# Kernel optimization log

Hardware: AMD Instinct MI355X
Metric: run time of the kernel (lower is better)

The kernel has to match this reference:

```python
import jax, jax.numpy as jnp
import numpy as np

B, S, E, H = 4, 2048, 1024, 16
D = E // H  # head_dim


def setup_inputs() -> dict:
    key = jax.random.key(0)
    ks = jax.random.split(key, 5)
    scale = 1.0 / np.sqrt(E)
    return {
        "qkv": jax.random.normal(ks[0], (B, S, E), jnp.float32),
        "in_w": jax.random.normal(ks[1], (3 * E, E), jnp.float32) * scale,
        "in_b": jax.random.normal(ks[2], (3 * E,), jnp.float32) * scale,
        "out_w": jax.random.normal(ks[3], (E, E), jnp.float32) * scale,
        "out_b": jax.random.normal(ks[4], (E,), jnp.float32) * scale,
    }


def reference(qkv, in_w, in_b, out_w, out_b):
    # in_proj: torch Linear -> x @ W^T + b, output [B,S,3E]
    x1 = jnp.einsum('bse,fe->bsf', qkv, in_w) + in_b
    q, k, v = jnp.split(x1, 3, axis=2)  # each [B,S,E]
    # reshape to heads: [B,H,S,D] (contiguous head_dim slices == reshape)
    q = q.reshape(B, S, H, D).transpose(0, 2, 1, 3)
    k = k.reshape(B, S, H, D).transpose(0, 2, 1, 3)
    v = v.reshape(B, S, H, D).transpose(0, 2, 1, 3)
    scores = jnp.einsum('bhqd,bhkd->bhqk', q, k) / jnp.sqrt(jnp.float32(D))
    attn = jax.nn.softmax(scores, axis=-1)  # dropout p=0.0 -> identity
    out = jnp.einsum('bhqk,bhkd->bhqd', attn, v)  # [B,H,S,D]
    out = out.transpose(0, 2, 1, 3).reshape(B, S, E)
    return jnp.einsum('bse,fe->bsf', out, out_w) + out_b
```

## Files before the change

### kernel.cpp

```cpp
#include <hip/hip_runtime.h>


typedef __attribute__((ext_vector_type(8))) short s16x8;
typedef __attribute__((ext_vector_type(8))) __bf16 bf16x8;
typedef __attribute__((ext_vector_type(4))) float f32x4;
typedef __attribute__((ext_vector_type(16))) float f32x16;
typedef __attribute__((ext_vector_type(4))) unsigned short u16x4;
typedef __attribute__((ext_vector_type(4))) unsigned int u32x4;

#define QSCALE_F 0.18033688011112042f

#if __has_builtin(__builtin_amdgcn_exp2f)
#define EXP2F(x) __builtin_amdgcn_exp2f(x)
#else
#define EXP2F(x) exp2f(x)
#endif

__device__ __forceinline__ unsigned short f2bf(float f) {
  unsigned int u = __builtin_bit_cast(unsigned int, f);
  u += 0x7fffu + ((u >> 16) & 1u);
  return (unsigned short)(u >> 16);
}

__device__ __forceinline__ f32x4 mfma16(s16x8 a, s16x8 b, f32x4 c) {
  return __builtin_amdgcn_mfma_f32_16x16x32_bf16(
      __builtin_bit_cast(bf16x8, a), __builtin_bit_cast(bf16x8, b), c, 0, 0, 0);
}
__device__ __forceinline__ f32x16 mfma32(s16x8 a, s16x8 b, f32x16 c) {
  return __builtin_amdgcn_mfma_f32_32x32x16_bf16(
      __builtin_bit_cast(bf16x8, a), __builtin_bit_cast(bf16x8, b), c, 0, 0, 0);
}

__device__ __forceinline__ unsigned cvtpk(float lo, float hi) {
  unsigned r;
  asm("v_cvt_pk_bf16_f32 %0, %1, %2" : "=v"(r) : "v"(lo), "v"(hi));
  return r;
}
__device__ __forceinline__ void p32swap(unsigned &a, unsigned &b) {
  asm volatile("v_permlane32_swap_b32 %0, %1" : "+v"(a), "+v"(b));
}

#define GLL16(gp, lp) __builtin_amdgcn_global_load_lds(                       \
    (const __attribute__((address_space(1))) void*)(gp),                      \
    (__attribute__((address_space(3))) void*)(lp), 16, 0, 0)

#define SBAR0 __builtin_amdgcn_sched_barrier(0)
#define HWBAR __builtin_amdgcn_s_barrier()
#define LGKM0 asm volatile("s_waitcnt lgkmcnt(0)" ::: "memory")
#define VMC4 asm volatile("s_waitcnt vmcnt(4)" ::: "memory")
#define VMC0 asm volatile("s_waitcnt vmcnt(0)" ::: "memory")
#define PRIO1 __builtin_amdgcn_s_setprio(1)
#define PRIO0 __builtin_amdgcn_s_setprio(0)

__global__ void cvt_f32_bf16(const float* __restrict__ in,
                             unsigned short* __restrict__ out,
                             int n, int scale_n) {
  int idx = (blockIdx.x * 256 + threadIdx.x) * 4;
  int stride = gridDim.x * 256 * 4;
  for (int i = idx; i < n; i += stride) {
    const float4 v = *reinterpret_cast<const float4*>(in + i);
    const float sc = (i < scale_n) ? QSCALE_F : 1.0f;
    u16x4 r;
    r.x = f2bf(v.x * sc); r.y = f2bf(v.y * sc);
    r.z = f2bf(v.z * sc); r.w = f2bf(v.w * sc);
    *reinterpret_cast<u16x4*>(out + i) = r;
  }
}

__global__ __launch_bounds__(512, 2) void gemm1_8ph(
    const unsigned short* __restrict__ A, const unsigned short* __restrict__ B,
    const float* __restrict__ bias, unsigned short* __restrict__ C,
    int M, int N, int K, int qscale_cols) {
  __shared__ __align__(16) unsigned short As[2][256 * 64];
  __shared__ __align__(16) unsigned short Bs[2][256 * 64];
  const int NT = K >> 6;
  const int id = blockIdx.x;
  const int mi_ = (id & 7) * 4 + ((id >> 3) & 3);
  const int ni_ = id >> 5;
  const int bm = mi_ * 256, bn = ni_ * 256;

  const int tid = threadIdx.x;
  const int lane = tid & 63, w = tid >> 6;
  const int l15 = lane & 15, l4 = (lane >> 4) & 3;
  const int wm = w >> 2, wn = w & 3;
  const int swz = (l15 & 7) << 4;

#define STG_HALF(ldsc_, gb_, ktel_) {                                         \
    _Pragma("unroll") for (int s_ = 0; s_ < 2; ++s_) {                        \
      const int o = (w * 2 + s_) * 1024 + lane * 16;                          \
      const int row_ = o >> 7;                                                \
      const int cb_ = (o & 127) ^ ((row_ & 7) << 4);                          \
      GLL16((gb_) + (size_t)row_ * K + (ktel_) + (cb_ >> 1),                  \
            (char*)(ldsc_) + o);                                              \
    }                                                                         \
  }
#define RD_A(buf_, qm_, dst_) {                                               \
    _Pragma("unroll") for (int mt = 0; mt < 4; ++mt)                          \
      _Pragma("unroll") for (int kk = 0; kk < 2; ++kk)                        \
        dst_[mt][kk] = *(const s16x8*)((const char*)As[buf_] +                \
            (wm * 128 + (qm_) * 64 + mt * 16 + l15) * 128 +                   \
            ((kk * 64 + l4 * 16) ^ swz));                                     \
  }
#define RD_B(buf_, qn_, dst_) {                                               \
    _Pragma("unroll") for (int nt = 0; nt < 2; ++nt)                          \
      _Pragma("unroll") for (int kk = 0; kk < 2; ++kk)                        \
        dst_[nt][kk] = *(const s16x8*)((const char*)Bs[buf_] +                \
            (wn * 64 + (qn_) * 32 + nt * 16 + l15) * 128 +                    \
            ((kk * 64 + l4 * 16) ^ swz));                                     \
  }
#define MMQ(qm_, qn_, a_, b_) {                                               \
    _Pragma("unroll") for (int mt = 0; mt < 4; ++mt)                          \
      _Pragma("unroll") for (int nt = 0; nt < 2; ++nt)                        \
        _Pragma("unroll") for (int kk = 0; kk < 2; ++kk)                      \
          acc[(qm_) * 4 + mt][(qn_) * 2 + nt] = mfma16(                       \
              a_[mt][kk], b_[nt][kk], acc[(qm_) * 4 + mt][(qn_) * 2 + nt]);   \
  }

  f32x4 acc[8][4];
#pragma unroll
  for (int i = 0; i < 8; ++i)
#pragma unroll
    for (int j = 0; j < 4; ++j) acc[i][j] = (f32x4){0.f, 0.f, 0.f, 0.f};

  const unsigned short* Ah0 = A + (size_t)bm * K;
  const unsigned short* Ah1 = A + (size_t)(bm + 128) * K;
  const unsigned short* Bh0 = B + (size_t)bn * K;
  const unsigned short* Bh1 = B + (size_t)(bn + 128) * K;

  STG_HALF(Bs[0], Bh0, 0);
  STG_HALF(As[0], Ah0, 0);
  STG_HALF((char*)Bs[0] + 16384, Bh1, 0);
  STG_HALF((char*)As[0] + 16384, Ah1, 0);
  STG_HALF(Bs[1], Bh0, 64);
  STG_HALF(As[1], Ah0, 64);
  VMC4;
  SBAR0; HWBAR;

  s16x8 a[4][2], b0[2][2], b1[2][2];
  for (int t = 0; t < NT; ++t) {
    const int cur = t & 1, oth = cur ^ 1;
    RD_A(cur, 0, a);
    RD_B(cur, 0, b0);
    if (t + 1 < NT) STG_HALF((char*)Bs[oth] + 16384, Bh1, (t + 1) * 64);
    SBAR0; HWBAR; LGKM0; SBAR0;
    PRIO1; MMQ(0, 0, a, b0); PRIO0;
    SBAR0; HWBAR;
    RD_B(cur, 1, b1);
    if (t + 1 < NT) STG_HALF((char*)As[oth] + 16384, Ah1, (t + 1) * 64);
    SBAR0; HWBAR; LGKM0; SBAR0;
    PRIO1; MMQ(0, 1, a, b1); PRIO0;
    SBAR0; HWBAR;
    RD_A(cur, 1, a);
    if (t + 2 < NT) STG_HALF(Bs[cur], Bh0, (t + 2) * 64);
    SBAR0; HWBAR; LGKM0; SBAR0;
    PRIO1; MMQ(1, 1, a, b1); PRIO0;
    SBAR0; HWBAR;
    if (t + 2 < NT) STG_HALF(As[cur], Ah0, (t + 2) * 64);
    SBAR0; HWBAR;
    PRIO1; MMQ(1, 0, a, b0); PRIO0;
    SBAR0;
    if (t + 2 < NT) { VMC4; } else { VMC0; }
    HWBAR;
  }

#pragma unroll
  for (int mi = 0; mi < 8; ++mi)
#pragma unroll
    for (int ni = 0; ni < 4; ++ni) {
      const int col = bn + wn * 64 + ni * 16 + l15;
      const float bsc = (col < qscale_cols) ? QSCALE_F : 1.0f;
      const float bv = bias[col] * bsc;
#pragma unroll
      for (int r = 0; r < 4; ++r) {
        const int row = bm + wm * 128 + mi * 16 + l4 * 4 + r;
        C[(size_t)row * N + col] = f2bf(acc[mi][ni][r] + bv);
      }
    }
#undef STG_HALF
#undef RD_A
#undef RD_B
#undef MMQ
}

template <bool OUT_BF16>
__global__ __launch_bounds__(256, 2) void gemm_nt(
    const unsigned short* __restrict__ A, const unsigned short* __restrict__ B,
    const float* __restrict__ bias, void* __restrict__ Cout,
    int M, int N, int K, int qscale_cols) {
  __shared__ __align__(16) unsigned short As[128 * 64];
  __shared__ __align__(16) unsigned short Bs[128 * 64];
  const int tid = threadIdx.x;
  const int lane = tid & 63, w = tid >> 6;
  const int l15 = lane & 15, l4 = lane >> 4;
  const int wr = w >> 1, wc = w & 1;
  const int bm = blockIdx.y * 128, bn = blockIdx.x * 128;

  f32x4 acc[4][4];
#pragma unroll
  for (int i = 0; i < 4; ++i)
#pragma unroll
    for (int j = 0; j < 4; ++j) acc[i][j] = (f32x4){0.f, 0.f, 0.f, 0.f};

  for (int kt = 0; kt < K; kt += 64) {
#pragma unroll
    for (int j = 0; j < 4; ++j) {
      const int gb = (j * 4 + w) * 64;
      const int g = gb + lane;
      const int row = g >> 3, seg = g & 7;
      GLL16(A + (size_t)(bm + row) * K + kt + seg * 8, As + gb * 8);
      GLL16(B + (size_t)(bn + row) * K + kt + seg * 8, Bs + gb * 8);
    }
    __syncthreads();
#pragma unroll
    for (int kk = 0; kk < 2; ++kk) {
      s16x8 a[4], b[4];
#pragma unroll
      for (int mi = 0; mi < 4; ++mi)
        a[mi] = *reinterpret_cast<const s16x8*>(
            As + (wr * 64 + mi * 16 + l15) * 64 + kk * 32 + l4 * 8);
#pragma unroll
      for (int ni = 0; ni < 4; ++ni)
        b[ni] = *reinterpret_cast<const s16x8*>(
            Bs + (wc * 64 + ni * 16 + l15) * 64 + kk * 32 + l4 * 8);
#pragma unroll
      for (int mi = 0; mi < 4; ++mi)
#pragma unroll
        for (int ni = 0; ni < 4; ++ni)
          acc[mi][ni] = mfma16(a[mi], b[ni], acc[mi][ni]);
    }
    __syncthreads();
  }
#pragma unroll
  for (int mi = 0; mi < 4; ++mi) {
#pragma unroll
    for (int ni = 0; ni < 4; ++ni) {
      const int col = bn + wc * 64 + ni * 16 + l15;
      const float bsc = (col < qscale_cols) ? QSCALE_F : 1.0f;
      const float bv = bias[col] * bsc;
#pragma unroll
      for (int r = 0; r < 4; ++r) {
        const int row = bm + wr * 64 + mi * 16 + l4 * 4 + r;
        const float val = acc[mi][ni][r] + bv;
        if (OUT_BF16)
          ((unsigned short*)Cout)[(size_t)row * N + col] = f2bf(val);
        else
          ((float*)Cout)[(size_t)row * N + col] = val;
      }
    }
  }
}

__global__ __launch_bounds__(256, 4) void attn_fwd(
    const unsigned short* __restrict__ X1, unsigned short* __restrict__ O) {
  __shared__ __align__(16) unsigned short Ks[2][64 * 64];
  __shared__ __align__(16) unsigned short Vt[2][64 * 64];

  const int id = blockIdx.x;
  const int xc = id & 7, r0 = id >> 3;
  const int bh = xc * 8 + (r0 & 7);
  const int qt = r0 >> 3;
  const int b = bh >> 4, h = bh & 15;
  const int tid = threadIdx.x;
  const int lane = tid & 63, w = tid >> 6;
  const int l31 = lane & 31, hi = lane >> 5;

  const unsigned short* Qp = X1 + (size_t)b * 2048 * 3072 + h * 64;
  const unsigned short* Kp = Qp + 1024;
  const unsigned short* Vp = Qp + 2048;
  const int q0 = qt * 128 + w * 32;

  s16x8 qf[4];
#pragma unroll
  for (int kk = 0; kk < 4; ++kk)
    qf[kk] = *reinterpret_cast<const s16x8*>(
        Qp + (size_t)(q0 + l31) * 3072 + kk * 16 + hi * 8);

  f32x16 oacc[2];
#pragma unroll
  for (int db = 0; db < 2; ++db)
#pragma unroll
    for (int i = 0; i < 16; ++i) oacc[db][i] = 0.f;
  float l_r = 0.f;

#define STAGE_K(kt_, buf_)                                                    \
  {                                                                           \
    _Pragma("unroll") for (int j = 0; j < 2; ++j) {                           \
      const int chunk = (j * 4 + w) * 1024;                                   \
      const int o = chunk + lane * 16;                                        \
      const int row = o >> 7;                                                 \
      const int srcb = (o & 127) ^ ((row & 7) << 4);                          \
      GLL16(Kp + (size_t)((kt_) + row) * 3072 + (srcb >> 1),                  \
            (char*)Ks[buf_] + chunk);                                         \
    }                                                                         \
  }
#define LOAD_V(kt_, vr_)                                                      \
  {                                                                           \
    _Pragma("unroll") for (int j = 0; j < 2; ++j) {                           \
      const int seg = w + 4 * j;                                              \
      vr_[j] = *reinterpret_cast<const s16x8*>(                               \
          Vp + (size_t)((kt_) + lane) * 3072 + seg * 8);                      \
    }                                                                         \
  }
#define WRITE_V(vr_, buf_)                                                    \
  {                                                                           \
    _Pragma("unroll") for (int j = 0; j < 2; ++j) {                           \
      const int seg = w + 4 * j;                                              \
      _Pragma("unroll") for (int e = 0; e < 8; ++e) {                         \
        const int d = seg * 8 + e;                                            \
        const int byt = d * 128 + ((lane * 2) ^ (e << 4));                    \
        *(unsigned short*)((char*)Vt[buf_] + byt) = (unsigned short)vr_[j][e];\
      }                                                                       \
    }                                                                         \
  }

  s16x8 vnxt[2];
  LOAD_V(0, vnxt);
  STAGE_K(0, 0);
  WRITE_V(vnxt, 0);
  __syncthreads();

  for (int t = 0; t < 32; ++t) {
    const int cur = t & 1;
    const unsigned short* Ksc = Ks[cur];
    const unsigned short* Vtc = Vt[cur];
    if (t < 31) {
      LOAD_V((t + 1) * 64, vnxt);
      STAGE_K((t + 1) * 64, cur ^ 1);
    }

    f32x16 sa[2];
#pragma unroll
    for (int sub = 0; sub < 2; ++sub)
#pragma unroll
      for (int i = 0; i < 16; ++i) sa[sub][i] = 0.f;
    PRIO1;
#pragma unroll
    for (int sub = 0; sub < 2; ++sub) {
      const int row = sub * 32 + l31;
#pragma unroll
      for (int kk = 0; kk < 4; ++kk) {
        const int byt = row * 128 + ((kk * 32 + hi * 16) ^ ((l31 & 7) << 4));
        s16x8 ka = *reinterpret_cast<const s16x8*>((const char*)Ksc + byt);
        sa[sub] = mfma32(ka, qf[kk], sa[sub]);
      }
    }
    PRIO0;

    float s0 = 0.f, s1 = 0.f, s2 = 0.f, s3 = 0.f;
#pragma unroll
    for (int sub = 0; sub < 2; ++sub)
#pragma unroll
      for (int i = 0; i < 16; i += 4) {
        sa[sub][i]     = EXP2F(sa[sub][i]);     s0 += sa[sub][i];
        sa[sub][i + 1] = EXP2F(sa[sub][i + 1]); s1 += sa[sub][i + 1];
        sa[sub][i + 2] = EXP2F(sa[sub][i + 2]); s2 += sa[sub][i + 2];
        sa[sub][i + 3] = EXP2F(sa[sub][i + 3]); s3 += sa[sub][i + 3];
      }
    float rsum = (s0 + s1) + (s2 + s3);
    rsum += __shfl_xor(rsum, 32);
    l_r += rsum;

    s16x8 pa[2][2];
#pragma unroll
    for (int sub = 0; sub < 2; ++sub)
#pragma unroll
      for (int g = 0; g < 2; ++g) {
        unsigned c0 = cvtpk(sa[sub][g * 8 + 0], sa[sub][g * 8 + 1]);
        unsigned c1 = cvtpk(sa[sub][g * 8 + 2], sa[sub][g * 8 + 3]);
        unsigned c2 = cvtpk(sa[sub][g * 8 + 4], sa[sub][g * 8 + 5]);
        unsigned c3 = cvtpk(sa[sub][g * 8 + 6], sa[sub][g * 8 + 7]);
        p32swap(c0, c2);
        p32swap(c1, c3);
        u32x4 tt = {c0, c1, c2, c3};
        pa[sub][g] = __builtin_bit_cast(s16x8, tt);
      }

    PRIO1;
#pragma unroll
    for (int db = 0; db < 2; ++db) {
      const int row = db * 32 + l31;
#pragma unroll
      for (int sub = 0; sub < 2; ++sub)
#pragma unroll
        for (int g = 0; g < 2; ++g) {
          const int byt =
              row * 128 + (((sub * 2 + g) * 32 + hi * 16) ^ ((l31 & 7) << 4));
          s16x8 vb = *reinterpret_cast<const s16x8*>((const char*)Vtc + byt);
          oacc[db] = mfma32(pa[sub][g], vb, oacc[db]);
        }
    }
    PRIO0;

    if (t < 31) WRITE_V(vnxt, cur ^ 1);
    __syncthreads();
  }

  const float invl = 1.0f / l_r;
#pragma unroll
  for (int r = 0; r < 16; ++r) {
    const int crow = (r & 3) + 8 * (r >> 2) + 4 * hi;
    const float ir = __shfl(invl, crow);
    const size_t base = (size_t)(b * 2048 + q0 + crow) * 1024 + h * 64 + l31;
    O[base] = f2bf(oacc[0][r] * ir);
    O[base + 32] = f2bf(oacc[1][r] * ir);
  }
}

extern "C" void kernel_launch(void* const* d_in, const int* in_sizes, int n_in,
                              void* d_out, int out_size, void* d_ws,
                              size_t ws_size, hipStream_t stream) {
  const float* qkv   = (const float*)d_in[0];
  const float* in_w  = (const float*)d_in[1];
  const float* in_b  = (const float*)d_in[2];
  const float* out_w = (const float*)d_in[3];
  const float* out_b = (const float*)d_in[4];
  float* out = (float*)d_out;
  char* ws = (char*)d_ws;

  unsigned short* qkv_bf  = (unsigned short*)(ws);
  unsigned short* win_bf  = (unsigned short*)(ws + 16777216);
  unsigned short* wout_bf = (unsigned short*)(ws + 23068672);
  unsigned short* x1      = (unsigned short*)(ws + 25165824);
  unsigned short* attn_out = qkv_bf;

  cvt_f32_bf16<<<2048, 256, 0, stream>>>(qkv, qkv_bf, 8388608, 0);
  cvt_f32_bf16<<<1024, 256, 0, stream>>>(in_w, win_bf, 3145728, 1048576);
  cvt_f32_bf16<<<512, 256, 0, stream>>>(out_w, wout_bf, 1048576, 0);

  gemm1_8ph<<<384, 512, 0, stream>>>(
      qkv_bf, win_bf, in_b, x1, 8192, 3072, 1024, 1024);

  attn_fwd<<<1024, 256, 0, stream>>>(x1, attn_out);

  gemm_nt<false><<<dim3(8, 64), 256, 0, stream>>>(
      attn_out, wout_bf, out_b, (void*)out, 8192, 1024, 1024, 0);
}
```

Measured before the change: 197.7 us.

## Retile QKV projection GEMM to 256x192 tiles with revised load pipeline

Changes the in-projection GEMM tile from 256x256 to 256x192, giving 512 blocks instead of 384 so the grid spreads more evenly across the CUs. The B shared-memory buffer shrinks, each wave now covers 48 columns, and global-to-LDS staging is rewritten as per-unit loads with a new vmcnt wait schedule inside the phase loop. Smaller tiles lower arithmetic intensity and add pipeline complexity in exchange for better occupancy and wave balance.

```diff
diff --git a/kernel.cpp b/kernel.cpp
--- a/kernel.cpp
+++ b/kernel.cpp
@@ -47,7 +47,8 @@
 #define SBAR0 __builtin_amdgcn_sched_barrier(0)
 #define HWBAR __builtin_amdgcn_s_barrier()
 #define LGKM0 asm volatile("s_waitcnt lgkmcnt(0)" ::: "memory")
-#define VMC4 asm volatile("s_waitcnt vmcnt(4)" ::: "memory")
+#define VMC5 asm volatile("s_waitcnt vmcnt(5)" ::: "memory")
+#define VMC2 asm volatile("s_waitcnt vmcnt(2)" ::: "memory")
 #define VMC0 asm volatile("s_waitcnt vmcnt(0)" ::: "memory")
 #define PRIO1 __builtin_amdgcn_s_setprio(1)
 #define PRIO0 __builtin_amdgcn_s_setprio(0)
@@ -72,12 +73,13 @@
     const float* __restrict__ bias, unsigned short* __restrict__ C,
     int M, int N, int K, int qscale_cols) {
   __shared__ __align__(16) unsigned short As[2][256 * 64];
-  __shared__ __align__(16) unsigned short Bs[2][256 * 64];
+  __shared__ __align__(16) unsigned short Bs[2][192 * 64];
   const int NT = K >> 6;
   const int id = blockIdx.x;
-  const int mi_ = (id & 7) * 4 + ((id >> 3) & 3);
-  const int ni_ = id >> 5;
-  const int bm = mi_ * 256, bn = ni_ * 256;
+  const int xc = id & 7, r0 = id >> 3;
+  const int mi_ = xc * 4 + (r0 & 3);
+  const int ni_ = r0 >> 2;
+  const int bm = mi_ * 256, bn = ni_ * 192;
 
   const int tid = threadIdx.x;
   const int lane = tid & 63, w = tid >> 6;
@@ -85,14 +87,12 @@
   const int wm = w >> 2, wn = w & 3;
   const int swz = (l15 & 7) << 4;
 
-#define STG_HALF(ldsc_, gb_, ktel_) {                                         \
-    _Pragma("unroll") for (int s_ = 0; s_ < 2; ++s_) {                        \
-      const int o = (w * 2 + s_) * 1024 + lane * 16;                          \
-      const int row_ = o >> 7;                                                \
-      const int cb_ = (o & 127) ^ ((row_ & 7) << 4);                          \
-      GLL16((gb_) + (size_t)row_ * K + (ktel_) + (cb_ >> 1),                  \
-            (char*)(ldsc_) + o);                                              \
-    }                                                                         \
+#define STG_U(ldsc_, gb_, unit_, ktel_) {                                     \
+    const int o = (unit_) * 8192 + tid * 16;                                  \
+    const int row_ = o >> 7;                                                  \
+    const int cb_ = (o & 127) ^ ((row_ & 7) << 4);                            \
+    GLL16((gb_) + (size_t)row_ * K + (ktel_) + (cb_ >> 1),                    \
+          (char*)(ldsc_) + o);                                                \
   }
 #define RD_A(buf_, qm_, dst_) {                                               \
     _Pragma("unroll") for (int mt = 0; mt < 4; ++mt)                          \
@@ -101,73 +101,82 @@
             (wm * 128 + (qm_) * 64 + mt * 16 + l15) * 128 +                   \
             ((kk * 64 + l4 * 16) ^ swz));                                     \
   }
-#define RD_B(buf_, qn_, dst_) {                                               \
+#define RD_B01(buf_, dst_) {                                                  \
     _Pragma("unroll") for (int nt = 0; nt < 2; ++nt)                          \
       _Pragma("unroll") for (int kk = 0; kk < 2; ++kk)                        \
         dst_[nt][kk] = *(const s16x8*)((const char*)Bs[buf_] +                \
-            (wn * 64 + (qn_) * 32 + nt * 16 + l15) * 128 +                    \
+            (wn * 48 + nt * 16 + l15) * 128 +                                 \
             ((kk * 64 + l4 * 16) ^ swz));                                     \
   }
-#define MMQ(qm_, qn_, a_, b_) {                                               \
+#define RD_B2(buf_, dst_) {                                                   \
+    _Pragma("unroll") for (int kk = 0; kk < 2; ++kk)                          \
+      dst_[kk] = *(const s16x8*)((const char*)Bs[buf_] +                      \
+          (wn * 48 + 32 + l15) * 128 + ((kk * 64 + l4 * 16) ^ swz));          \
+  }
+#define MM16(qm_) {                                                           \
     _Pragma("unroll") for (int mt = 0; mt < 4; ++mt)                          \
       _Pragma("unroll") for (int nt = 0; nt < 2; ++nt)                        \
         _Pragma("unroll") for (int kk = 0; kk < 2; ++kk)                      \
-          acc[(qm_) * 4 + mt][(qn_) * 2 + nt] = mfma16(                       \
-              a_[mt][kk], b_[nt][kk], acc[(qm_) * 4 + mt][(qn_) * 2 + nt]);   \
-  }
-
-  f32x4 acc[8][4];
+          acc[(qm_) * 4 + mt][nt] = mfma16(                                   \
+              a[mt][kk], b01[nt][kk], acc[(qm_) * 4 + mt][nt]);               \
+  }
+#define MM8(qm_) {                                                            \
+    _Pragma("unroll") for (int mt = 0; mt < 4; ++mt)                          \
+      _Pragma("unroll") for (int kk = 0; kk < 2; ++kk)                        \
+        acc[(qm_) * 4 + mt][2] = mfma16(                                      \
+            a[mt][kk], b2[kk], acc[(qm_) * 4 + mt][2]);                       \
+  }
+
+  f32x4 acc[8][3];
 #pragma unroll
   for (int i = 0; i < 8; ++i)
 #pragma unroll
-    for (int j = 0; j < 4; ++j) acc[i][j] = (f32x4){0.f, 0.f, 0.f, 0.f};
-
-  const unsigned short* Ah0 = A + (size_t)bm * K;
-  const unsigned short* Ah1 = A + (size_t)(bm + 128) * K;
-  const unsigned short* Bh0 = B + (size_t)bn * K;
-  const unsigned short* Bh1 = B + (size_t)(bn + 128) * K;
-
-  STG_HALF(Bs[0], Bh0, 0);
-  STG_HALF(As[0], Ah0, 0);
-  STG_HALF((char*)Bs[0] + 16384, Bh1, 0);
-  STG_HALF((char*)As[0] + 16384, Ah1, 0);
-  STG_HALF(Bs[1], Bh0, 64);
-  STG_HALF(As[1], Ah0, 64);
-  VMC4;
+    for (int j = 0; j < 3; ++j) acc[i][j] = (f32x4){0.f, 0.f, 0.f, 0.f};
+
+  const unsigned short* Ag = A + (size_t)bm * K;
+  const unsigned short* Bg = B + (size_t)bn * K;
+
+  STG_U(Bs[0], Bg, 0, 0); STG_U(Bs[0], Bg, 1, 0); STG_U(Bs[0], Bg, 2, 0);
+  STG_U(As[0], Ag, 0, 0); STG_U(As[0], Ag, 2, 0);
+  STG_U(As[0], Ag, 1, 0); STG_U(As[0], Ag, 3, 0);
+  VMC0;
   SBAR0; HWBAR;
 
-  s16x8 a[4][2], b0[2][2], b1[2][2];
+  s16x8 a[4][2], b01[2][2], b2[2];
   for (int t = 0; t < NT; ++t) {
     const int cur = t & 1, oth = cur ^ 1;
+    const bool st = (t + 1 < NT);
+    const int kel = (t + 1) * 64;
     RD_A(cur, 0, a);
-    RD_B(cur, 0, b0);
-    if (t + 1 < NT) STG_HALF((char*)Bs[oth] + 16384, Bh1, (t + 1) * 64);
+    RD_B01(cur, b01);
+    if (st) { STG_U(Bs[oth], Bg, 0, kel); STG_U(Bs[oth], Bg, 1, kel);
+              STG_U(Bs[oth], Bg, 2, kel); }
     SBAR0; HWBAR; LGKM0; SBAR0;
-    PRIO1; MMQ(0, 0, a, b0); PRIO0;
+    PRIO1; MM16(0); PRIO0;
     SBAR0; HWBAR;
-    RD_B(cur, 1, b1);
-    if (t + 1 < NT) STG_HALF((char*)As[oth] + 16384, Ah1, (t + 1) * 64);
+    RD_B2(cur, b2);
+    if (st) { STG_U(As[oth], Ag, 0, kel); STG_U(As[oth], Ag, 2, kel); }
     SBAR0; HWBAR; LGKM0; SBAR0;
-    PRIO1; MMQ(0, 1, a, b1); PRIO0;
+    PRIO1; MM8(0); PRIO0;
+    SBAR0;
+    if (st) { VMC5; } else { VMC0; }
+    HWBAR;
+    RD_A(cur, 1, a);
+    if (st) { STG_U(As[oth], Ag, 1, kel); STG_U(As[oth], Ag, 3, kel); }
+    SBAR0; HWBAR; LGKM0; SBAR0;
+    PRIO1; MM8(1); PRIO0;
     SBAR0; HWBAR;
-    RD_A(cur, 1, a);
-    if (t + 2 < NT) STG_HALF(Bs[cur], Bh0, (t + 2) * 64);
-    SBAR0; HWBAR; LGKM0; SBAR0;
-    PRIO1; MMQ(1, 1, a, b1); PRIO0;
-    SBAR0; HWBAR;
-    if (t + 2 < NT) STG_HALF(As[cur], Ah0, (t + 2) * 64);
-    SBAR0; HWBAR;
-    PRIO1; MMQ(1, 0, a, b0); PRIO0;
+    PRIO1; MM16(1); PRIO0;
     SBAR0;
-    if (t + 2 < NT) { VMC4; } else { VMC0; }
+    if (st) { VMC2; } else { VMC0; }
     HWBAR;
   }
 
 #pragma unroll
   for (int mi = 0; mi < 8; ++mi)
 #pragma unroll
-    for (int ni = 0; ni < 4; ++ni) {
-      const int col = bn + wn * 64 + ni * 16 + l15;
+    for (int ni = 0; ni < 3; ++ni) {
+      const int col = bn + wn * 48 + ni * 16 + l15;
       const float bsc = (col < qscale_cols) ? QSCALE_F : 1.0f;
       const float bv = bias[col] * bsc;
 #pragma unroll
@@ -176,10 +185,12 @@
         C[(size_t)row * N + col] = f2bf(acc[mi][ni][r] + bv);
       }
     }
-#undef STG_HALF
+#undef STG_U
 #undef RD_A
-#undef RD_B
-#undef MMQ
+#undef RD_B01
+#undef RD_B2
+#undef MM16
+#undef MM8
 }
 
 template <bool OUT_BF16>
@@ -427,7 +438,7 @@
   cvt_f32_bf16<<<1024, 256, 0, stream>>>(in_w, win_bf, 3145728, 1048576);
   cvt_f32_bf16<<<512, 256, 0, stream>>>(out_w, wout_bf, 1048576, 0);
 
-  gemm1_8ph<<<384, 512, 0, stream>>>(
+  gemm1_8ph<<<512, 512, 0, stream>>>(
       qkv_bf, win_bf, in_b, x1, 8192, 3072, 1024, 1024);
 
   attn_fwd<<<1024, 256, 0, stream>>>(x1, attn_out);
```

New measurement: 190.6 us. 1.04x faster.
